# Optimization experiments

Measured on AMD Instinct MI355X. Metric: run time of the kernel, lower is better.

The kernel has to match this reference:

```python
import jax, jax.numpy as jnp
import numpy as np

HID, HEADS, FF, DEPTH = 1152, 16, 4304, 2
HD = HID // HEADS            # 72
ROT = HD // 2                # 36 (rotary_pos_emb width)
S, NSEG = 2048, 4
EPS = 1e-6


def _layernorm(x, w, b):
    m = jnp.mean(x, axis=-1, keepdims=True)
    xc = x - m
    v = jnp.mean(xc * xc, axis=-1, keepdims=True)
    return xc * jax.lax.rsqrt(v + EPS) * w + b


def _rotate_half(x):
    x1, x2 = jnp.split(x, 2, axis=-1)
    return jnp.concatenate([-x2, x1], axis=-1)


def _apply_rotary(t, freqs):
    # t: [S, H, D], freqs: [S, D/2]
    emb = jnp.concatenate([freqs, freqs], axis=-1)          # [S, D]
    cos = jnp.cos(emb)[:, None, :]
    sin = jnp.sin(emb)[:, None, :]
    return t * cos + _rotate_half(t) * sin


def setup_inputs() -> dict:
    key = jax.random.key(0)
    ks = jax.random.split(key, 16)
    sd = 0.02
    # rotary freqs as in VisionRotaryEmbedding(dim=HD//2): h-pos and w-pos halves
    inv_freq = 1.0 / (10000.0 ** (jnp.arange(0, ROT, 2, dtype=jnp.float32) / ROT))  # [18]
    pos = jnp.arange(S, dtype=jnp.float32)
    hpos, wpos = pos // 32.0, pos % 32.0
    rotary = jnp.concatenate([jnp.outer(hpos, inv_freq), jnp.outer(wpos, inv_freq)], axis=-1)  # [S, 36]
    return {
        "x": jax.random.normal(ks[0], (S, HID), jnp.float32),
        "cu_seqlens": jnp.arange(NSEG + 1, dtype=jnp.int32) * (S // NSEG),
        "rotary_pos_emb": rotary,
        "norm1_w": jnp.ones((DEPTH, HID), jnp.float32),
        "norm1_b": jnp.zeros((DEPTH, HID), jnp.float32),
        "qkv_w": jax.random.normal(ks[1], (DEPTH, 3 * HID, HID), jnp.float32) * sd,
        "qkv_b": jnp.zeros((DEPTH, 3 * HID), jnp.float32),
        "proj_w": jax.random.normal(ks[2], (DEPTH, HID, HID), jnp.float32) * sd,
        "proj_b": jnp.zeros((DEPTH, HID), jnp.float32),
        "norm2_w": jnp.ones((DEPTH, HID), jnp.float32),
        "norm2_b": jnp.zeros((DEPTH, HID), jnp.float32),
        "fc1_w": jax.random.normal(ks[3], (DEPTH, FF, HID), jnp.float32) * sd,
        "fc1_b": jnp.zeros((DEPTH, FF), jnp.float32),
        "fc2_w": jax.random.normal(ks[4], (DEPTH, HID, FF), jnp.float32) * sd,
        "fc2_b": jnp.zeros((DEPTH, HID), jnp.float32),
    }


def _forward(x, cu_seqlens, rotary_pos_emb, norm1_w, norm1_b, qkv_w, qkv_b,
             proj_w, proj_b, norm2_w, norm2_b, fc1_w, fc1_b, fc2_w, fc2_b):
    seq_len = x.shape[0]
    # block-diagonal additive mask from cu_seqlens (same mask the torch loop builds)
    seg = jnp.searchsorted(cu_seqlens, jnp.arange(seq_len, dtype=cu_seqlens.dtype), side="right") - 1
    same = seg[:, None] == seg[None, :]
    bias = jnp.where(same, jnp.float32(0.0), jnp.finfo(jnp.float32).min)  # [S, S]
    scale = 1.0 / np.sqrt(HD)
    for d in range(DEPTH):
        # --- attention ---
        h = _layernorm(x, norm1_w[d], norm1_b[d])
        qkv = (h @ qkv_w[d].T + qkv_b[d]).reshape(seq_len, 3, HEADS, HD)
        q, k, v = qkv[:, 0], qkv[:, 1], qkv[:, 2]           # [S, H, D]
        q = _apply_rotary(q, rotary_pos_emb)
        k = _apply_rotary(k, rotary_pos_emb)
        scores = jnp.einsum("qhd,khd->hqk", q, k) * scale + bias[None]
        probs = jax.nn.softmax(scores.astype(jnp.float32), axis=-1).astype(q.dtype)
        attn = jnp.einsum("hqk,khd->qhd", probs, v).reshape(seq_len, HID)
        x = x + attn @ proj_w[d].T + proj_b[d]
        # --- MLP (gelu tanh approx) ---
        h2 = _layernorm(x, norm2_w[d], norm2_b[d])
        x = x + jax.nn.gelu(h2 @ fc1_w[d].T + fc1_b[d], approximate=True) @ fc2_w[d].T + fc2_b[d]
    return x


def reference(x, cu_seqlens, rotary_pos_emb, norm1_w, norm1_b, qkv_w, qkv_b,
              proj_w, proj_b, norm2_w, norm2_b, fc1_w, fc1_b, fc2_w, fc2_b):
    return _forward(x, cu_seqlens, rotary_pos_emb, norm1_w, norm1_b, qkv_w, qkv_b,
                    proj_w, proj_b, norm2_w, norm2_b, fc1_w, fc1_b, fc2_w, fc2_b)
```

## Files before the change

kernel.cpp:

```cpp
#include <hip/hip_runtime.h>

#define S_LEN 2048
#define HID   1152
#define HEADS 16
#define HD    72
#define ROT   36
#define LD3   3456
#define FF    4304
#define FFP   4320

typedef short s16x8 __attribute__((ext_vector_type(8)));
typedef short s16x4 __attribute__((ext_vector_type(4)));
typedef float f32x4 __attribute__((ext_vector_type(4)));
typedef short bf_t;

__device__ __forceinline__ short f2b(float f) {
  unsigned u = __float_as_uint(f);
  u += 0x7fffu + ((u >> 16) & 1u);
  return (short)(u >> 16);
}
__device__ __forceinline__ float b2f(short h) {
  return __uint_as_float(((unsigned)(unsigned short)h) << 16);
}
__device__ __forceinline__ float gelu_f(float x) {
  float t = tanhf(0.7978845608028654f * (x + 0.044715f * x * x * x));
  return 0.5f * x * (1.0f + t);
}

typedef const __attribute__((address_space(1))) void* gas_p;
typedef __attribute__((address_space(3))) void* las_p;
__device__ __forceinline__ void gload16(const void* g, void* l) {
  __builtin_amdgcn_global_load_lds((gas_p)g, (las_p)l, 16, 0, 0);
}

#define QKV_OFF 0
#define P_OFF   (3456 * 1152)
#define F1_OFF  (P_OFF + 1152 * 1152)
#define F2_OFF  (F1_OFF + 4352 * 1152)
#define ARENA_ELEMS (F2_OFF + 1152 * 4320)
#define GA_Q  (8960 * 288)
#define TOT_Q (GA_Q + 1152 * 1080)

__global__ __launch_bounds__(256) void convw_all(
    const float* __restrict__ qkvw, const float* __restrict__ projw,
    const float* __restrict__ fc1w, const float* __restrict__ fc2w,
    bf_t* __restrict__ arena)
{
  int idx = blockIdx.x * 256 + threadIdx.x;
  if (idx >= TOT_Q) return;
  if (idx < GA_Q) {
    int row = idx / 288, kq = (idx % 288) * 4;
    const float* s = nullptr; bf_t* d;
    if (row < 3456)      { s = qkvw + (size_t)row * 1152;  d = arena + (size_t)row * 1152; }
    else if (row < 4608) { int r = row - 3456; s = projw + (size_t)r * 1152; d = arena + P_OFF + (size_t)r * 1152; }
    else                 { int r = row - 4608; d = arena + F1_OFF + (size_t)r * 1152;
                           if (r < FF) s = fc1w + (size_t)r * 1152; }
    s16x4 o;
    if (s) { float4 v = *(const float4*)(s + kq);
             o[0] = f2b(v.x); o[1] = f2b(v.y); o[2] = f2b(v.z); o[3] = f2b(v.w); }
    else   { o[0] = 0; o[1] = 0; o[2] = 0; o[3] = 0; }
    *(s16x4*)(d + kq) = o;
  } else {
    int q = idx - GA_Q;
    int r = q / 1080, kq = (q % 1080) * 4;
    s16x4 o;
    if (kq < FF) {
      float4 v = *(const float4*)(fc2w + (size_t)r * FF + kq);
      o[0] = f2b(v.x); o[1] = f2b(v.y); o[2] = f2b(v.z); o[3] = f2b(v.w);
    } else { o[0] = 0; o[1] = 0; o[2] = 0; o[3] = 0; }
    *(s16x4*)(arena + F2_OFF + (size_t)r * FFP + kq) = o;
  }
}

__global__ __launch_bounds__(256) void costab_kernel(
    const float* __restrict__ rot, float* __restrict__ ct, float* __restrict__ st)
{
  int i = blockIdx.x * 256 + threadIdx.x;
  if (i < S_LEN * ROT) { float f = rot[i]; ct[i] = cosf(f); st[i] = sinf(f); }
}

__global__ __launch_bounds__(256) void ln_kernel(
    const float* __restrict__ x, const float* __restrict__ wgt,
    const float* __restrict__ bia, bf_t* __restrict__ outb)
{
  const int row = blockIdx.x, tid = threadIdx.x;
  const float4* xr = (const float4*)(x + (size_t)row * HID);
  float4 a = xr[tid];
  float4 b2 = make_float4(0.f, 0.f, 0.f, 0.f);
  const bool has2 = tid < 32;
  if (has2) b2 = xr[256 + tid];
  float s = a.x + a.y + a.z + a.w + b2.x + b2.y + b2.z + b2.w;
  float q = a.x*a.x + a.y*a.y + a.z*a.z + a.w*a.w
          + b2.x*b2.x + b2.y*b2.y + b2.z*b2.z + b2.w*b2.w;
  for (int mk = 32; mk; mk >>= 1) { s += __shfl_xor(s, mk); q += __shfl_xor(q, mk); }
  __shared__ float red[16];
  if ((tid & 63) == 0) { red[tid >> 6] = s; red[8 + (tid >> 6)] = q; }
  __syncthreads();
  if (tid == 0) {
    red[4]  = red[0] + red[1] + red[2] + red[3];
    red[12] = red[8] + red[9] + red[10] + red[11];
  }
  __syncthreads();
  float mean = red[4] * (1.0f / HID);
  float var  = red[12] * (1.0f / HID) - mean * mean;
  float rstd = rsqrtf(var + 1e-6f);
  const float4* w4 = (const float4*)wgt;
  const float4* b4 = (const float4*)bia;
  s16x4* o4 = (s16x4*)(outb + (size_t)row * HID);
  {
    float4 wv = w4[tid], bv = b4[tid];
    s16x4 o;
    o[0] = f2b((a.x - mean) * rstd * wv.x + bv.x);
    o[1] = f2b((a.y - mean) * rstd * wv.y + bv.y);
    o[2] = f2b((a.z - mean) * rstd * wv.z + bv.z);
    o[3] = f2b((a.w - mean) * rstd * wv.w + bv.w);
    o4[tid] = o;
  }
  if (has2) {
    float4 wv = w4[256 + tid], bv = b4[256 + tid];
    s16x4 o;
    o[0] = f2b((b2.x - mean) * rstd * wv.x + bv.x);
    o[1] = f2b((b2.y - mean) * rstd * wv.y + bv.y);
    o[2] = f2b((b2.z - mean) * rstd * wv.z + bv.z);
    o[3] = f2b((b2.w - mean) * rstd * wv.w + bv.w);
    o4[256 + tid] = o;
  }
}

__global__ __launch_bounds__(256) void redln_kernel(
    const float* __restrict__ part, const float* __restrict__ bias,
    const float* __restrict__ resid, float* __restrict__ xout,
    bf_t* __restrict__ hout, const float* __restrict__ lnw,
    const float* __restrict__ lnb, int do_ln)
{
  const int row = blockIdx.x, tid = threadIdx.x;
  const size_t base = (size_t)row * 288;
  const float4* r4 = (const float4*)resid;
  const float4* b4 = (const float4*)bias;
  const float4* p4 = (const float4*)part;
  const bool has2 = tid < 32;

  float4 a, c;
  {
    float4 r = r4[base + tid], bv = b4[tid];
    a = make_float4(r.x + bv.x, r.y + bv.y, r.z + bv.z, r.w + bv.w);
#pragma unroll
    for (int p = 0; p < 4; p++) {
      float4 v = p4[(size_t)p * S_LEN * 288 + base + tid];
      a.x += v.x; a.y += v.y; a.z += v.z; a.w += v.w;
    }
  }
  c = make_float4(0.f, 0.f, 0.f, 0.f);
  if (has2) {
    float4 r = r4[base + 256 + tid], bv = b4[256 + tid];
    c = make_float4(r.x + bv.x, r.y + bv.y, r.z + bv.z, r.w + bv.w);
#pragma unroll
    for (int p = 0; p < 4; p++) {
      float4 v = p4[(size_t)p * S_LEN * 288 + base + 256 + tid];
      c.x += v.x; c.y += v.y; c.z += v.z; c.w += v.w;
    }
  }
  ((float4*)xout)[base + tid] = a;
  if (has2) ((float4*)xout)[base + 256 + tid] = c;

  if (!do_ln) return;

  float s = a.x + a.y + a.z + a.w + c.x + c.y + c.z + c.w;
  float q = a.x*a.x + a.y*a.y + a.z*a.z + a.w*a.w
          + c.x*c.x + c.y*c.y + c.z*c.z + c.w*c.w;
  for (int mk = 32; mk; mk >>= 1) { s += __shfl_xor(s, mk); q += __shfl_xor(q, mk); }
  __shared__ float red[16];
  if ((tid & 63) == 0) { red[tid >> 6] = s; red[8 + (tid >> 6)] = q; }
  __syncthreads();
  if (tid == 0) {
    red[4]  = red[0] + red[1] + red[2] + red[3];
    red[12] = red[8] + red[9] + red[10] + red[11];
  }
  __syncthreads();
  float mean = red[4] * (1.0f / HID);
  float var  = red[12] * (1.0f / HID) - mean * mean;
  float rstd = rsqrtf(var + 1e-6f);
  const float4* w4 = (const float4*)lnw;
  const float4* lb4 = (const float4*)lnb;
  s16x4* o4 = (s16x4*)(hout + (size_t)row * HID);
  {
    float4 wv = w4[tid], bv = lb4[tid];
    s16x4 o;
    o[0] = f2b((a.x - mean) * rstd * wv.x + bv.x);
    o[1] = f2b((a.y - mean) * rstd * wv.y + bv.y);
    o[2] = f2b((a.z - mean) * rstd * wv.z + bv.z);
    o[3] = f2b((a.w - mean) * rstd * wv.w + bv.w);
    o4[tid] = o;
  }
  if (has2) {
    float4 wv = w4[256 + tid], bv = lb4[256 + tid];
    s16x4 o;
    o[0] = f2b((c.x - mean) * rstd * wv.x + bv.x);
    o[1] = f2b((c.y - mean) * rstd * wv.y + bv.y);
    o[2] = f2b((c.z - mean) * rstd * wv.z + bv.z);
    o[3] = f2b((c.w - mean) * rstd * wv.w + bv.w);
    o4[256 + tid] = o;
  }
}

__global__ __launch_bounds__(256) void rotary_kernel(
    bf_t* __restrict__ qkv, const float* __restrict__ ct, const float* __restrict__ st)
{
  int idx = blockIdx.x * 256 + threadIdx.x;
  if (idx >= S_LEN * HEADS * ROT) return;
  int t = idx / (HEADS * ROT);
  int r = idx % (HEADS * ROT);
  int h = r / ROT, dd = r % ROT;
  float c = ct[t * ROT + dd], s = st[t * ROT + dd];
  size_t base = (size_t)t * LD3 + h * HD + dd;
  float q1 = b2f(qkv[base]),        q2 = b2f(qkv[base + ROT]);
  float k1 = b2f(qkv[base + HID]),  k2 = b2f(qkv[base + HID + ROT]);
  const float scale = 0.11785113019775793f;
  qkv[base]             = f2b((q1 * c - q2 * s) * scale);
  qkv[base + ROT]       = f2b((q2 * c + q1 * s) * scale);
  qkv[base + HID]       = f2b(k1 * c - k2 * s);
  qkv[base + HID + ROT] = f2b(k2 * c + k1 * s);
}

template<int MODE>
__global__ __launch_bounds__(256, 4) void gemm1(
    const bf_t* __restrict__ A, int lda,
    const bf_t* __restrict__ B, int ldb,
    const float* __restrict__ bias, int nbias,
    void* outp, int ldc, int nvalid, int K, int kchunk)
{
  __shared__ __align__(16) bf_t As[128 * 32];
  __shared__ __align__(16) bf_t Bs[128 * 32];
  const int tid = threadIdx.x;
  const int l = tid & 63, w = tid >> 6;
  const int lr = l & 15, lg = l >> 4;
  const int wm = (w >> 1) * 64, wn = (w & 1) * 64;

  unsigned gx = gridDim.x, gy = gridDim.y, gz = gridDim.z;
  unsigned nwg = gx * gy * gz;
  unsigned lin = (blockIdx.z * gy + blockIdx.y) * gx + blockIdx.x;
  if ((nwg & 7u) == 0u) {
    unsigned q = nwg >> 3;
    lin = (lin & 7u) * q + (lin >> 3);
  }
  const unsigned bz = lin / (gx * gy);
  const unsigned rem = lin % (gx * gy);
  const unsigned by = rem / gx, bx = rem % gx;

  const int rowA0 = by * 128, colB0 = bx * 128;
  const int kb0 = bz * kchunk;
  int kb1 = kb0 + kchunk; if (kb1 > K) kb1 = K;

  const int o1 = tid * 16, o2 = o1 + 4096;
  const int r1 = o1 >> 6, c1 = o1 & 63;
  const int r2 = o2 >> 6, c2 = o2 & 63;
  const char* Ab = (const char*)A;
  const char* Bb = (const char*)B;

  f32x4 acc[4][4] = {};

  for (int kb = kb0; kb < kb1; kb += 32) {
    gload16(Ab + ((size_t)(rowA0 + r1) * lda + kb) * 2 + c1, (char*)As + o1);
    gload16(Ab + ((size_t)(rowA0 + r2) * lda + kb) * 2 + c2, (char*)As + o2);
    gload16(Bb + ((size_t)(colB0 + r1) * ldb + kb) * 2 + c1, (char*)Bs + o1);
    gload16(Bb + ((size_t)(colB0 + r2) * ldb + kb) * 2 + c2, (char*)Bs + o2);
    asm volatile("s_waitcnt vmcnt(0)" ::: "memory");
    __syncthreads();
    s16x8 af[4], bv[4];
#pragma unroll
    for (int mt = 0; mt < 4; mt++) af[mt] = *(const s16x8*)&As[(wm + mt * 16 + lr) * 32 + lg * 8];
#pragma unroll
    for (int nt = 0; nt < 4; nt++) bv[nt] = *(const s16x8*)&Bs[(wn + nt * 16 + lr) * 32 + lg * 8];
#pragma unroll
    for (int mt = 0; mt < 4; mt++)
#pragma unroll
      for (int nt = 0; nt < 4; nt++)
        acc[mt][nt] = __builtin_amdgcn_mfma_f32_16x16x32_bf16(af[mt], bv[nt], acc[mt][nt], 0, 0, 0);
    __syncthreads();
  }

#pragma unroll
  for (int mt = 0; mt < 4; mt++) {
    const int rr = rowA0 + wm + mt * 16 + lg * 4;
#pragma unroll
    for (int nt = 0; nt < 4; nt++) {
      const int cc = colB0 + wn + nt * 16 + lr;
      const float bvl = (MODE == 3) ? 0.0f : ((cc < nbias) ? bias[cc] : 0.0f);
#pragma unroll
      for (int i = 0; i < 4; i++) {
        float v = acc[mt][nt][i] + bvl;
        const int row = rr + i;
        if (MODE == 0) {
          ((bf_t*)outp)[(size_t)row * ldc + cc] = f2b(v);
        } else if (MODE == 2) {
          if (cc < nvalid)      ((bf_t*)outp)[(size_t)row * ldc + cc] = f2b(gelu_f(v));
          else if (cc < ldc)    ((bf_t*)outp)[(size_t)row * ldc + cc] = 0;
        } else {
          float* P = (float*)outp + (size_t)bz * ((size_t)S_LEN * ldc);
          P[(size_t)row * ldc + cc] = v;
        }
      }
    }
  }
}

template<int MODE>
__global__ __launch_bounds__(256, 4) void gemm2(
    const bf_t* __restrict__ A, int lda,
    const bf_t* __restrict__ B, int ldb,
    const float* __restrict__ bias, int nbias,
    void* outp, int ldc, int nvalid, int K, int kchunk)
{
  __shared__ __align__(16) bf_t As[2][128 * 32];
  __shared__ __align__(16) bf_t Bs[2][64 * 32];
  const int tid = threadIdx.x;
  const int l = tid & 63, w = tid >> 6;
  const int lr = l & 15, lg = l >> 4;
  const int wm = (w >> 1) * 64, wn = (w & 1) * 32;

  unsigned gx = gridDim.x, gy = gridDim.y, gz = gridDim.z;
  unsigned nwg = gx * gy * gz;
  unsigned lin = (blockIdx.z * gy + blockIdx.y) * gx + blockIdx.x;
  if ((nwg & 7u) == 0u) {
    unsigned q = nwg >> 3;
    lin = (lin & 7u) * q + (lin >> 3);
  }
  const unsigned bz = lin / (gx * gy);
  const unsigned rem = lin % (gx * gy);
  const unsigned by = rem / gx, bx = rem % gx;

  const int rowA0 = by * 128, colB0 = bx * 64;
  const int kb0 = bz * kchunk;
  int kb1 = kb0 + kchunk; if (kb1 > K) kb1 = K;

  const int oA1 = tid * 16, oA2 = oA1 + 4096;
  const int rA1 = oA1 >> 6, cA1 = oA1 & 63;
  const int rA2 = rA1 + 64;
  const int oB = tid * 16;
  const int rB = oB >> 6, cB = oB & 63;
  const char* Ab = (const char*)A;
  const char* Bb = (const char*)B;

#define STAGE(buf, kk) do { \
    gload16(Ab + ((size_t)(rowA0 + rA1) * lda + (kk)) * 2 + cA1, (char*)As[buf] + oA1); \
    gload16(Ab + ((size_t)(rowA0 + rA2) * lda + (kk)) * 2 + cA1, (char*)As[buf] + oA2); \
    gload16(Bb + ((size_t)(colB0 + rB)  * ldb + (kk)) * 2 + cB,  (char*)Bs[buf] + oB);  \
  } while (0)

  f32x4 acc[4][2] = {};

  STAGE(0, kb0);
  asm volatile("s_waitcnt vmcnt(0)" ::: "memory");
  __builtin_amdgcn_s_barrier();
  __builtin_amdgcn_sched_barrier(0);

  int cur = 0;
  for (int kb = kb0; kb < kb1; kb += 32) {
    if (kb + 32 < kb1) STAGE(cur ^ 1, kb + 32);
    s16x8 af[4], bv[2];
#pragma unroll
    for (int mt = 0; mt < 4; mt++)
      af[mt] = *(const s16x8*)&As[cur][(wm + mt * 16 + lr) * 32 + lg * 8];
#pragma unroll
    for (int nt = 0; nt < 2; nt++)
      bv[nt] = *(const s16x8*)&Bs[cur][(wn + nt * 16 + lr) * 32 + lg * 8];
    asm volatile("s_waitcnt lgkmcnt(0)" ::: "memory");
    __builtin_amdgcn_sched_barrier(0);
#pragma unroll
    for (int mt = 0; mt < 4; mt++)
#pragma unroll
      for (int nt = 0; nt < 2; nt++)
        acc[mt][nt] = __builtin_amdgcn_mfma_f32_16x16x32_bf16(af[mt], bv[nt], acc[mt][nt], 0, 0, 0);
    asm volatile("s_waitcnt vmcnt(0)" ::: "memory");
    __builtin_amdgcn_s_barrier();
    __builtin_amdgcn_sched_barrier(0);
    cur ^= 1;
  }
#undef STAGE

#pragma unroll
  for (int mt = 0; mt < 4; mt++) {
    const int rr = rowA0 + wm + mt * 16 + lg * 4;
#pragma unroll
    for (int nt = 0; nt < 2; nt++) {
      const int cc = colB0 + wn + nt * 16 + lr;
      const float bvl = (cc < nbias) ? bias[cc] : 0.0f;
#pragma unroll
      for (int i = 0; i < 4; i++) {
        float v = acc[mt][nt][i] + bvl;
        const int row = rr + i;
        if (MODE == 0) {
          ((bf_t*)outp)[(size_t)row * ldc + cc] = f2b(v);
        } else if (MODE == 2) {
          if (cc < nvalid)      ((bf_t*)outp)[(size_t)row * ldc + cc] = f2b(gelu_f(v));
          else if (cc < ldc)    ((bf_t*)outp)[(size_t)row * ldc + cc] = 0;
        } else {
          float* P = (float*)outp + (size_t)bz * ((size_t)S_LEN * ldc);
          P[(size_t)row * ldc + cc] = v;
        }
      }
    }
  }
}

#define QSTR 104
#define VSTR 76
#define PSTR 72
__global__ __launch_bounds__(256, 2) void attn_kernel(
    const bf_t* __restrict__ qkv, const int* __restrict__ cu, int nseg,
    bf_t* __restrict__ outb)
{
  __shared__ __align__(16) bf_t Qs[64 * QSTR];
  __shared__ __align__(16) bf_t Ks[2][64 * QSTR];
  __shared__ __align__(16) bf_t VTs[2][80 * VSTR];
  __shared__ __align__(16) bf_t Pb[4][16 * PSTR];
  const int tid = threadIdx.x;
  const int l = tid & 63, w = tid >> 6;
  const int lr = l & 15, lg = l >> 4;
  const int h = blockIdx.y;
  const int qbase = blockIdx.x * 64;

  int kstart = 0, kend = S_LEN;
  for (int s2 = 0; s2 < nseg; s2++) {
    int a = cu[s2], b = cu[s2 + 1];
    if (qbase >= a && qbase < b) { kstart = a; kend = b; }
  }

  for (int i = tid; i < 64 * QSTR; i += 256)
    if ((i % QSTR) >= HD) { Qs[i] = 0; Ks[0][i] = 0; Ks[1][i] = 0; }
  for (int i = tid; i < 80 * VSTR; i += 256)
    if ((i / VSTR) >= HD) { VTs[0][i] = 0; VTs[1][i] = 0; }
  for (int c = tid; c < 576; c += 256) {
    int r = c / 9, j = c % 9;
    *(s16x8*)&Qs[r * QSTR + j * 8] =
        *(const s16x8*)&qkv[(size_t)(qbase + r) * LD3 + h * HD + j * 8];
  }
  {
#pragma unroll
    for (int u = 0; u < 3; u++) {
      int c = tid + u * 256;
      if (c < 576) {
        int r = c / 9, j = c % 9;
        int gr = kstart + r; if (gr >= kend) gr = kend - 1;
        *(s16x8*)&Ks[0][r * QSTR + j * 8] =
            *(const s16x8*)&qkv[(size_t)gr * LD3 + HID + h * HD + j * 8];
      }
    }
#pragma unroll
    for (int u = 0; u < 3; u++) {
      int c = tid + u * 256;
      if (c < 576) {
        int r = c & 63, j = c >> 6;
        int gr = kstart + r; if (gr >= kend) gr = kend - 1;
        s16x8 v = *(const s16x8*)&qkv[(size_t)gr * LD3 + 2 * HID + h * HD + j * 8];
#pragma unroll
        for (int jj = 0; jj < 8; jj++) VTs[0][(j * 8 + jj) * VSTR + r] = v[jj];
      }
    }
  }
  __syncthreads();

  s16x8 qf[3];
#pragma unroll
  for (int ks = 0; ks < 3; ks++)
    qf[ks] = *(const s16x8*)&Qs[(w * 16 + lr) * QSTR + ks * 32 + lg * 8];

  float m_i[4], l_i[4];
  f32x4 Of[5] = {};
#pragma unroll
  for (int i = 0; i < 4; i++) { m_i[i] = -1e30f; l_i[i] = 0.0f; }

  const int ntile = (kend - kstart + 63) >> 6;
  int cur = 0;
  for (int t = 0; t < ntile; t++) {
    const int kb = kstart + t * 64;
    const bool more = (t + 1 < ntile);

    s16x8 kreg[3], vreg[3];
    if (more) {
      const int nb = kb + 64;
#pragma unroll
      for (int u = 0; u < 3; u++) {
        int c = tid + u * 256;
        if (c < 576) {
          int r = c / 9, j = c % 9;
          int gr = nb + r; if (gr >= kend) gr = kend - 1;
          kreg[u] = *(const s16x8*)&qkv[(size_t)gr * LD3 + HID + h * HD + j * 8];
        }
      }
#pragma unroll
      for (int u = 0; u < 3; u++) {
        int c = tid + u * 256;
        if (c < 576) {
          int r = c & 63, j = c >> 6;
          int gr = nb + r; if (gr >= kend) gr = kend - 1;
          vreg[u] = *(const s16x8*)&qkv[(size_t)gr * LD3 + 2 * HID + h * HD + j * 8];
        }
      }
    }

    f32x4 sc[4] = {};
#pragma unroll
    for (int kc = 0; kc < 4; kc++) {
#pragma unroll
      for (int ks = 0; ks < 3; ks++) {
        s16x8 kf = *(const s16x8*)&Ks[cur][(kc * 16 + lr) * QSTR + ks * 32 + lg * 8];
        sc[kc] = __builtin_amdgcn_mfma_f32_16x16x32_bf16(qf[ks], kf, sc[kc], 0, 0, 0);
      }
    }
#pragma unroll
    for (int kc = 0; kc < 4; kc++) {
      if ((kb + kc * 16 + lr) >= kend) {
#pragma unroll
        for (int i = 0; i < 4; i++) sc[kc][i] = -1e30f;
      }
    }
    float tmax[4], scl[4], rs[4];
#pragma unroll
    for (int i = 0; i < 4; i++) {
      float tm = fmaxf(fmaxf(sc[0][i], sc[1][i]), fmaxf(sc[2][i], sc[3][i]));
#pragma unroll
      for (int d2 = 1; d2 < 16; d2 <<= 1) tm = fmaxf(tm, __shfl_xor(tm, d2));
      tmax[i] = tm;
    }
#pragma unroll
    for (int i = 0; i < 4; i++) {
      float mn = fmaxf(m_i[i], tmax[i]);
      scl[i] = __expf(m_i[i] - mn);
      m_i[i] = mn;
      rs[i] = 0.0f;
    }
#pragma unroll
    for (int kc = 0; kc < 4; kc++)
#pragma unroll
      for (int i = 0; i < 4; i++) {
        float p = __expf(sc[kc][i] - m_i[i]);
        sc[kc][i] = p;
        rs[i] += p;
      }
#pragma unroll
    for (int i = 0; i < 4; i++) {
#pragma unroll
      for (int d2 = 1; d2 < 16; d2 <<= 1) rs[i] += __shfl_xor(rs[i], d2);
      l_i[i] = l_i[i] * scl[i] + rs[i];
    }
#pragma unroll
    for (int nt = 0; nt < 5; nt++)
#pragma unroll
      for (int i = 0; i < 4; i++) Of[nt][i] *= scl[i];
#pragma unroll
    for (int kc = 0; kc < 4; kc++)
#pragma unroll
      for (int i = 0; i < 4; i++)
        Pb[w][(lg * 4 + i) * PSTR + kc * 16 + lr] = f2b(sc[kc][i]);
    asm volatile("s_waitcnt lgkmcnt(0)" ::: "memory");
    __builtin_amdgcn_sched_barrier(0);
    s16x8 pf[2];
#pragma unroll
    for (int k2 = 0; k2 < 2; k2++)
      pf[k2] = *(const s16x8*)&Pb[w][lr * PSTR + k2 * 32 + lg * 8];
#pragma unroll
    for (int nt = 0; nt < 5; nt++) {
#pragma unroll
      for (int k2 = 0; k2 < 2; k2++) {
        const int vb = (nt * 16 + lr) * VSTR + k2 * 32 + lg * 8;
        s16x4 va = *(const s16x4*)&VTs[cur][vb];
        s16x4 vb2 = *(const s16x4*)&VTs[cur][vb + 4];
        s16x8 vf;
        vf[0] = va[0]; vf[1] = va[1]; vf[2] = va[2]; vf[3] = va[3];
        vf[4] = vb2[0]; vf[5] = vb2[1]; vf[6] = vb2[2]; vf[7] = vb2[3];
        Of[nt] = __builtin_amdgcn_mfma_f32_16x16x32_bf16(pf[k2], vf, Of[nt], 0, 0, 0);
      }
    }

    if (more) {
#pragma unroll
      for (int u = 0; u < 3; u++) {
        int c = tid + u * 256;
        if (c < 576) {
          int r = c / 9, j = c % 9;
          *(s16x8*)&Ks[cur ^ 1][r * QSTR + j * 8] = kreg[u];
        }
      }
#pragma unroll
      for (int u = 0; u < 3; u++) {
        int c = tid + u * 256;
        if (c < 576) {
          int r = c & 63, j = c >> 6;
#pragma unroll
          for (int jj = 0; jj < 8; jj++)
            VTs[cur ^ 1][(j * 8 + jj) * VSTR + r] = vreg[u][jj];
        }
      }
    }
    __syncthreads();
    cur ^= 1;
  }

  float inv[4];
#pragma unroll
  for (int i = 0; i < 4; i++) inv[i] = 1.0f / l_i[i];
#pragma unroll
  for (int nt = 0; nt < 5; nt++) {
    int cc = nt * 16 + lr;
    if (cc < HD) {
#pragma unroll
      for (int i = 0; i < 4; i++) {
        int row = qbase + w * 16 + lg * 4 + i;
        outb[(size_t)row * HID + h * HD + cc] = f2b(Of[nt][i] * inv[i]);
      }
    }
  }
}

extern "C" void kernel_launch(void* const* d_in, const int* in_sizes, int n_in,
                              void* d_out, int out_size, void* d_ws, size_t ws_size,
                              hipStream_t stream) {
  const float* x     = (const float*)d_in[0];
  const int*   cu    = (const int*)d_in[1];
  const float* rotab = (const float*)d_in[2];
  const float* n1w   = (const float*)d_in[3];
  const float* n1b   = (const float*)d_in[4];
  const float* qkvw  = (const float*)d_in[5];
  const float* qkvb  = (const float*)d_in[6];
  const float* projw = (const float*)d_in[7];
  const float* projb = (const float*)d_in[8];
  const float* n2w   = (const float*)d_in[9];
  const float* n2b   = (const float*)d_in[10];
  const float* fc1w  = (const float*)d_in[11];
  const float* fc1b  = (const float*)d_in[12];
  const float* fc2w  = (const float*)d_in[13];
  const float* fc2b  = (const float*)d_in[14];
  float* out = (float*)d_out;
  char* ws = (char*)d_ws;

  size_t off = 0;
  float* xbuf = (float*)(ws + off); off += (size_t)S_LEN * HID * 4;
  bf_t* hbf   = (bf_t*)(ws + off);  off += (size_t)S_LEN * HID * 2;
  bf_t* qkvbf = (bf_t*)(ws + off);
  bf_t* ff1bf = (bf_t*)(ws + off);  off += (size_t)S_LEN * FFP * 2;
  bf_t* attnbf= (bf_t*)(ws + off);  off += (size_t)S_LEN * HID * 2;
  bf_t* arena = (bf_t*)(ws + off);  off += (size_t)ARENA_ELEMS * 2;
  float* ctab = (float*)(ws + off); off += (size_t)S_LEN * ROT * 4;
  float* stab = (float*)(ws + off); off += (size_t)S_LEN * ROT * 4;
  float* part = (float*)(ws + off); off += (size_t)4 * S_LEN * HID * 4;

  costab_kernel<<<(S_LEN * ROT + 255) / 256, 256, 0, stream>>>(rotab, ctab, stab);

  const int nseg = in_sizes[1] - 1;

  for (int d = 0; d < 2; d++) {
    const float* xin = (d == 0) ? x : xbuf;
    convw_all<<<(TOT_Q + 255) / 256, 256, 0, stream>>>(
        qkvw + (size_t)d * LD3 * HID, projw + (size_t)d * HID * HID,
        fc1w + (size_t)d * FF * HID, fc2w + (size_t)d * HID * FF, arena);
    if (d == 0)
      ln_kernel<<<S_LEN, 256, 0, stream>>>(x, n1w, n1b, hbf);
    gemm2<0><<<dim3(LD3 / 64, 16), 256, 0, stream>>>(
        hbf, HID, arena + QKV_OFF, HID, qkvb + (size_t)d * LD3, LD3,
        qkvbf, LD3, LD3, HID, HID);
    rotary_kernel<<<(S_LEN * HEADS * ROT + 255) / 256, 256, 0, stream>>>(qkvbf, ctab, stab);
    attn_kernel<<<dim3(S_LEN / 64, HEADS), 256, 0, stream>>>(qkvbf, cu, nseg, attnbf);
    gemm1<3><<<dim3(HID / 128, 16, 4), 256, 0, stream>>>(
        attnbf, HID, arena + P_OFF, HID, nullptr, 0, part, HID, HID, HID, 288);
    redln_kernel<<<S_LEN, 256, 0, stream>>>(
        part, projb + (size_t)d * HID, xin, xbuf, hbf,
        n2w + (size_t)d * HID, n2b + (size_t)d * HID, 1);
    gemm2<2><<<dim3((FFP + 63) / 64, 16), 256, 0, stream>>>(
        hbf, HID, arena + F1_OFF, HID, fc1b + (size_t)d * FF, FF,
        ff1bf, FFP, FF, HID, HID);
    gemm1<3><<<dim3(HID / 128, 16, 4), 256, 0, stream>>>(
        ff1bf, FFP, arena + F2_OFF, FFP, nullptr, 0, part, HID, HID, FFP, 1088);
    if (d == 0) {
      redln_kernel<<<S_LEN, 256, 0, stream>>>(
          part, fc2b, xbuf, xbuf, hbf, n1w + HID, n1b + HID, 1);
    } else {
      redln_kernel<<<S_LEN, 256, 0, stream>>>(
          part, fc2b + (size_t)HID, xbuf, out, nullptr, nullptr, nullptr, 0);
    }
  }
}
```

Measured before the change: 410.8 us.

## Replace QKV and FC1 GEMMs with 256x256-tile 8-wave double-buffered kernel

Adds a gemm8p kernel with 256x256 output tiles, 512 threads, a K step of 64, XOR-swizzled LDS and double-buffered global-to-LDS prefetch interleaved with MFMA phases, using s_setprio to favour the MFMA blocks. It is used for the QKV and FC1 projections in place of the 128x64 gemm2. The weight arena and FFP padding are enlarged to multiples of 256 so that the full tiles stay in bounds, and gemm1 is reduced to the partial-sum output path only. The larger tiles cut global and LDS traffic per FLOP but give a small grid (112 and 136 blocks) with 128 KB of LDS per block, which risks poor CU occupancy.

```diff
diff --git a/kernel.cpp b/kernel.cpp
--- a/kernel.cpp
+++ b/kernel.cpp
@@ -7,7 +7,7 @@
 #define ROT   36
 #define LD3   3456
 #define FF    4304
-#define FFP   4320
+#define FFP   4352
 
 typedef short s16x8 __attribute__((ext_vector_type(8)));
 typedef short s16x4 __attribute__((ext_vector_type(4)));
@@ -34,12 +34,12 @@
 }
 
 #define QKV_OFF 0
-#define P_OFF   (3456 * 1152)
+#define P_OFF   (3584 * 1152)
 #define F1_OFF  (P_OFF + 1152 * 1152)
 #define F2_OFF  (F1_OFF + 4352 * 1152)
-#define ARENA_ELEMS (F2_OFF + 1152 * 4320)
-#define GA_Q  (8960 * 288)
-#define TOT_Q (GA_Q + 1152 * 1080)
+#define ARENA_ELEMS (F2_OFF + 1152 * 4352)
+#define GA_Q  (9088 * 288)
+#define TOT_Q (GA_Q + 1152 * 1088)
 
 __global__ __launch_bounds__(256) void convw_all(
     const float* __restrict__ qkvw, const float* __restrict__ projw,
@@ -51,9 +51,11 @@
   if (idx < GA_Q) {
     int row = idx / 288, kq = (idx % 288) * 4;
     const float* s = nullptr; bf_t* d;
-    if (row < 3456)      { s = qkvw + (size_t)row * 1152;  d = arena + (size_t)row * 1152; }
-    else if (row < 4608) { int r = row - 3456; s = projw + (size_t)r * 1152; d = arena + P_OFF + (size_t)r * 1152; }
-    else                 { int r = row - 4608; d = arena + F1_OFF + (size_t)r * 1152;
+    if (row < 3584)      { if (row < 3456) s = qkvw + (size_t)row * 1152;
+                           d = arena + (size_t)row * 1152; }
+    else if (row < 4736) { int r = row - 3584; s = projw + (size_t)r * 1152;
+                           d = arena + P_OFF + (size_t)r * 1152; }
+    else                 { int r = row - 4736; d = arena + F1_OFF + (size_t)r * 1152;
                            if (r < FF) s = fc1w + (size_t)r * 1152; }
     s16x4 o;
     if (s) { float4 v = *(const float4*)(s + kq);
@@ -62,7 +64,7 @@
     *(s16x4*)(d + kq) = o;
   } else {
     int q = idx - GA_Q;
-    int r = q / 1080, kq = (q % 1080) * 4;
+    int r = q / 1088, kq = (q % 1088) * 4;
     s16x4 o;
     if (kq < FF) {
       float4 v = *(const float4*)(fc2w + (size_t)r * FF + kq);
@@ -223,6 +225,125 @@
 }
 
 template<int MODE>
+__global__ __launch_bounds__(512, 2) void gemm8p(
+    const bf_t* __restrict__ A, int lda,
+    const bf_t* __restrict__ B, int ldb,
+    const float* __restrict__ bias, int nbias,
+    void* outp, int ldc, int nvalid, int K)
+{
+  __shared__ __align__(16) char smem[131072];
+  const int tid = threadIdx.x;
+  const int l = tid & 63, w = tid >> 6;
+  const int lr = l & 15, lg = l >> 4;
+  const int wr = w >> 2, wc = w & 3;
+
+  unsigned gx = gridDim.x, gy = gridDim.y;
+  unsigned nwg = gx * gy;
+  unsigned lin = blockIdx.y * gx + blockIdx.x;
+  if ((nwg & 7u) == 0u) { unsigned q = nwg >> 3; lin = (lin & 7u) * q + (lin >> 3); }
+  const unsigned by = lin / gx, bx = lin % gx;
+  const int rowA0 = by * 256, colB0 = bx * 256;
+
+  const char* Ab = (const char*)A;
+  const char* Bb = (const char*)B;
+  const int rS = tid >> 3;
+  const int cS = ((tid & 7) * 16) ^ (((tid >> 5) & 1) << 5);
+
+  auto stage_half = [&](int nb, int mat, int h, int kb) {
+#pragma unroll
+    for (int j = 0; j < 2; j++) {
+      const char* src;
+      if (mat == 0) {
+        int row = rowA0 + h * 128 + j * 64 + rS;
+        src = Ab + ((size_t)row * lda + kb) * 2 + cS;
+      } else {
+        int row = colB0 + h * 128 + j * 64 + rS;
+        src = Bb + ((size_t)row * ldb + kb) * 2 + cS;
+      }
+      char* dst = (char*)smem + mat * 65536 + (nb * 2 + h) * 16384 + j * 8192 + tid * 16;
+      gload16(src, dst);
+    }
+  };
+
+  f32x4 acc[8][4] = {};
+
+  stage_half(0, 0, 0, 0); stage_half(0, 0, 1, 0);
+  stage_half(0, 1, 0, 0); stage_half(0, 1, 1, 0);
+  asm volatile("s_waitcnt vmcnt(0)" ::: "memory");
+  __builtin_amdgcn_s_barrier();
+
+  const int ntk = K >> 6;
+  const int swz = ((lr >> 2) & 1) << 5;
+  for (int T = 0; T < ntk; T++) {
+    const int buf = T & 1;
+    const int nb = buf ^ 1;
+    const bool pre = (T + 1 < ntk);
+    const int kb1 = (T + 1) << 6;
+    const char* Abase = (const char*)smem + (buf * 2 + wr) * 16384;
+    const char* Bbase = (const char*)smem + 65536 + (buf * 2 + (wc >> 1)) * 16384;
+#pragma unroll
+    for (int q = 0; q < 4; q++) {
+      const int qm = q >> 1, qn = q & 1;
+      s16x8 af[4][2], bv[2][2];
+#pragma unroll
+      for (int ks = 0; ks < 2; ks++) {
+        const int cb = (ks * 64 + lg * 16) ^ swz;
+#pragma unroll
+        for (int mi = 0; mi < 4; mi++) {
+          const int rowin = (qm * 4 + mi) * 16 + lr;
+          af[mi][ks] = *(const s16x8*)(Abase + rowin * 128 + cb);
+        }
+#pragma unroll
+        for (int ni = 0; ni < 2; ni++) {
+          const int rowin = (wc & 1) * 64 + (qn * 2 + ni) * 16 + lr;
+          bv[ni][ks] = *(const s16x8*)(Bbase + rowin * 128 + cb);
+        }
+      }
+      if (pre) {
+        if (q == 0)      { stage_half(nb, 0, 0, kb1); stage_half(nb, 0, 1, kb1); }
+        else if (q == 1) { stage_half(nb, 1, 0, kb1); stage_half(nb, 1, 1, kb1); }
+      }
+      asm volatile("s_waitcnt lgkmcnt(0)" ::: "memory");
+      __builtin_amdgcn_sched_barrier(0);
+      __builtin_amdgcn_s_setprio(1);
+#pragma unroll
+      for (int ks = 0; ks < 2; ks++)
+#pragma unroll
+        for (int mi = 0; mi < 4; mi++)
+#pragma unroll
+          for (int ni = 0; ni < 2; ni++)
+            acc[qm * 4 + mi][qn * 2 + ni] =
+              __builtin_amdgcn_mfma_f32_16x16x32_bf16(
+                  af[mi][ks], bv[ni][ks], acc[qm * 4 + mi][qn * 2 + ni], 0, 0, 0);
+      __builtin_amdgcn_s_setprio(0);
+      if (q == 3 && pre) asm volatile("s_waitcnt vmcnt(0)" ::: "memory");
+      __builtin_amdgcn_s_barrier();
+    }
+  }
+
+#pragma unroll
+  for (int m = 0; m < 8; m++) {
+    const int row = rowA0 + wr * 128 + m * 16 + lg * 4;
+#pragma unroll
+    for (int n = 0; n < 4; n++) {
+      const int cc = colB0 + wc * 64 + n * 16 + lr;
+      if (cc >= ldc) continue;
+      const float bvl = (cc < nbias) ? bias[cc] : 0.0f;
+#pragma unroll
+      for (int i = 0; i < 4; i++) {
+        float v = acc[m][n][i] + bvl;
+        if (MODE == 0) {
+          if (cc < nvalid) ((bf_t*)outp)[(size_t)(row + i) * ldc + cc] = f2b(v);
+        } else {
+          if (cc < nvalid) ((bf_t*)outp)[(size_t)(row + i) * ldc + cc] = f2b(gelu_f(v));
+          else             ((bf_t*)outp)[(size_t)(row + i) * ldc + cc] = 0;
+        }
+      }
+    }
+  }
+}
+
+template<int MODE>
 __global__ __launch_bounds__(256, 4) void gemm1(
     const bf_t* __restrict__ A, int lda,
     const bf_t* __restrict__ B, int ldb,
@@ -285,119 +406,11 @@
 #pragma unroll
     for (int nt = 0; nt < 4; nt++) {
       const int cc = colB0 + wn + nt * 16 + lr;
-      const float bvl = (MODE == 3) ? 0.0f : ((cc < nbias) ? bias[cc] : 0.0f);
 #pragma unroll
       for (int i = 0; i < 4; i++) {
-        float v = acc[mt][nt][i] + bvl;
         const int row = rr + i;
-        if (MODE == 0) {
-          ((bf_t*)outp)[(size_t)row * ldc + cc] = f2b(v);
-        } else if (MODE == 2) {
-          if (cc < nvalid)      ((bf_t*)outp)[(size_t)row * ldc + cc] = f2b(gelu_f(v));
-          else if (cc < ldc)    ((bf_t*)outp)[(size_t)row * ldc + cc] = 0;
-        } else {
-          float* P = (float*)outp + (size_t)bz * ((size_t)S_LEN * ldc);
-          P[(size_t)row * ldc + cc] = v;
-        }
-      }
-    }
-  }
-}
-
-template<int MODE>
-__global__ __launch_bounds__(256, 4) void gemm2(
-    const bf_t* __restrict__ A, int lda,
-    const bf_t* __restrict__ B, int ldb,
-    const float* __restrict__ bias, int nbias,
-    void* outp, int ldc, int nvalid, int K, int kchunk)
-{
-  __shared__ __align__(16) bf_t As[2][128 * 32];
-  __shared__ __align__(16) bf_t Bs[2][64 * 32];
-  const int tid = threadIdx.x;
-  const int l = tid & 63, w = tid >> 6;
-  const int lr = l & 15, lg = l >> 4;
-  const int wm = (w >> 1) * 64, wn = (w & 1) * 32;
-
-  unsigned gx = gridDim.x, gy = gridDim.y, gz = gridDim.z;
-  unsigned nwg = gx * gy * gz;
-  unsigned lin = (blockIdx.z * gy + blockIdx.y) * gx + blockIdx.x;
-  if ((nwg & 7u) == 0u) {
-    unsigned q = nwg >> 3;
-    lin = (lin & 7u) * q + (lin >> 3);
-  }
-  const unsigned bz = lin / (gx * gy);
-  const unsigned rem = lin % (gx * gy);
-  const unsigned by = rem / gx, bx = rem % gx;
-
-  const int rowA0 = by * 128, colB0 = bx * 64;
-  const int kb0 = bz * kchunk;
-  int kb1 = kb0 + kchunk; if (kb1 > K) kb1 = K;
-
-  const int oA1 = tid * 16, oA2 = oA1 + 4096;
-  const int rA1 = oA1 >> 6, cA1 = oA1 & 63;
-  const int rA2 = rA1 + 64;
-  const int oB = tid * 16;
-  const int rB = oB >> 6, cB = oB & 63;
-  const char* Ab = (const char*)A;
-  const char* Bb = (const char*)B;
-
-#define STAGE(buf, kk) do { \
-    gload16(Ab + ((size_t)(rowA0 + rA1) * lda + (kk)) * 2 + cA1, (char*)As[buf] + oA1); \
-    gload16(Ab + ((size_t)(rowA0 + rA2) * lda + (kk)) * 2 + cA1, (char*)As[buf] + oA2); \
-    gload16(Bb + ((size_t)(colB0 + rB)  * ldb + (kk)) * 2 + cB,  (char*)Bs[buf] + oB);  \
-  } while (0)
-
-  f32x4 acc[4][2] = {};
-
-  STAGE(0, kb0);
-  asm volatile("s_waitcnt vmcnt(0)" ::: "memory");
-  __builtin_amdgcn_s_barrier();
-  __builtin_amdgcn_sched_barrier(0);
-
-  int cur = 0;
-  for (int kb = kb0; kb < kb1; kb += 32) {
-    if (kb + 32 < kb1) STAGE(cur ^ 1, kb + 32);
-    s16x8 af[4], bv[2];
-#pragma unroll
-    for (int mt = 0; mt < 4; mt++)
-      af[mt] = *(const s16x8*)&As[cur][(wm + mt * 16 + lr) * 32 + lg * 8];
-#pragma unroll
-    for (int nt = 0; nt < 2; nt++)
-      bv[nt] = *(const s16x8*)&Bs[cur][(wn + nt * 16 + lr) * 32 + lg * 8];
-    asm volatile("s_waitcnt lgkmcnt(0)" ::: "memory");
-    __builtin_amdgcn_sched_barrier(0);
-#pragma unroll
-    for (int mt = 0; mt < 4; mt++)
-#pragma unroll
-      for (int nt = 0; nt < 2; nt++)
-        acc[mt][nt] = __builtin_amdgcn_mfma_f32_16x16x32_bf16(af[mt], bv[nt], acc[mt][nt], 0, 0, 0);
-    asm volatile("s_waitcnt vmcnt(0)" ::: "memory");
-    __builtin_amdgcn_s_barrier();
-    __builtin_amdgcn_sched_barrier(0);
-    cur ^= 1;
-  }
-#undef STAGE
-
-#pragma unroll
-  for (int mt = 0; mt < 4; mt++) {
-    const int rr = rowA0 + wm + mt * 16 + lg * 4;
-#pragma unroll
-    for (int nt = 0; nt < 2; nt++) {
-      const int cc = colB0 + wn + nt * 16 + lr;
-      const float bvl = (cc < nbias) ? bias[cc] : 0.0f;
-#pragma unroll
-      for (int i = 0; i < 4; i++) {
-        float v = acc[mt][nt][i] + bvl;
-        const int row = rr + i;
-        if (MODE == 0) {
-          ((bf_t*)outp)[(size_t)row * ldc + cc] = f2b(v);
-        } else if (MODE == 2) {
-          if (cc < nvalid)      ((bf_t*)outp)[(size_t)row * ldc + cc] = f2b(gelu_f(v));
-          else if (cc < ldc)    ((bf_t*)outp)[(size_t)row * ldc + cc] = 0;
-        } else {
-          float* P = (float*)outp + (size_t)bz * ((size_t)S_LEN * ldc);
-          P[(size_t)row * ldc + cc] = v;
-        }
+        float* P = (float*)outp + (size_t)bz * ((size_t)S_LEN * ldc);
+        P[(size_t)row * ldc + cc] = acc[mt][nt][i];
       }
     }
   }
@@ -656,9 +669,9 @@
         fc1w + (size_t)d * FF * HID, fc2w + (size_t)d * HID * FF, arena);
     if (d == 0)
       ln_kernel<<<S_LEN, 256, 0, stream>>>(x, n1w, n1b, hbf);
-    gemm2<0><<<dim3(LD3 / 64, 16), 256, 0, stream>>>(
+    gemm8p<0><<<dim3(14, 8), 512, 0, stream>>>(
         hbf, HID, arena + QKV_OFF, HID, qkvb + (size_t)d * LD3, LD3,
-        qkvbf, LD3, LD3, HID, HID);
+        qkvbf, LD3, LD3, HID);
     rotary_kernel<<<(S_LEN * HEADS * ROT + 255) / 256, 256, 0, stream>>>(qkvbf, ctab, stab);
     attn_kernel<<<dim3(S_LEN / 64, HEADS), 256, 0, stream>>>(qkvbf, cu, nseg, attnbf);
     gemm1<3><<<dim3(HID / 128, 16, 4), 256, 0, stream>>>(
@@ -666,9 +679,9 @@
     redln_kernel<<<S_LEN, 256, 0, stream>>>(
         part, projb + (size_t)d * HID, xin, xbuf, hbf,
         n2w + (size_t)d * HID, n2b + (size_t)d * HID, 1);
-    gemm2<2><<<dim3((FFP + 63) / 64, 16), 256, 0, stream>>>(
+    gemm8p<2><<<dim3(17, 8), 512, 0, stream>>>(
         hbf, HID, arena + F1_OFF, HID, fc1b + (size_t)d * FF, FF,
-        ff1bf, FFP, FF, HID, HID);
+        ff1bf, FFP, FF, HID);
     gemm1<3><<<dim3(HID / 128, 16, 4), 256, 0, stream>>>(
         ff1bf, FFP, arena + F2_OFF, FFP, nullptr, 0, part, HID, HID, FFP, 1088);
     if (d == 0) {
```

After: 581.4 us. 41.5% more time.
